# Performance work log

Measured on AMD Instinct MI355X. Metric: run time of the kernel, lower is better.

Reference implementation:

```python
import jax, jax.numpy as jnp
import numpy as np

B = 65536
IN_F = 1024
OUT_F = 1024


def setup_inputs() -> dict:
    key = jax.random.key(0)
    k1, k2 = jax.random.split(key)
    x = jax.random.normal(k1, (B, IN_F), dtype=jnp.float32)
    # init matches torch: normal(0, sqrt(2/(in+out)))
    std = np.sqrt(2.0 / (IN_F + OUT_F)).astype(np.float32)
    weight = jax.random.normal(k2, (OUT_F, IN_F), dtype=jnp.float32) * std
    bias = jnp.zeros((OUT_F,), dtype=jnp.float32)
    return {"x": x, "weight": weight, "bias": bias}


def reference(x, weight, bias):
    # Deterministic binarization: sign(w) in {-1, 0, +1} (sign(0)=0, same as torch)
    w_bin = jnp.sign(weight)
    # [B, in] @ [in, out] + [out]
    return jnp.matmul(x, w_bin.T) + bias[None, :]
```

## Files before the change

### kernel.cpp

```cpp
#include <hip/hip_runtime.h>


typedef __bf16 bf16x8 __attribute__((ext_vector_type(8)));
typedef __bf16 bf16x4 __attribute__((ext_vector_type(4)));
typedef float  f32x4  __attribute__((ext_vector_type(4)));

constexpr int Mdim = 65536, Ndim = 1024, Kdim = 1024;
constexpr int BM = 256, BN = 256, BK = 64;
constexpr int NKT = Kdim / BK;
constexpr int NWG = (Mdim / BM) * (Ndim / BN);

typedef const __attribute__((address_space(1))) char ga_char;
typedef __attribute__((address_space(3))) char lds_char;
__device__ __forceinline__ void gload16(const void* g, void* l) {
    __builtin_amdgcn_global_load_lds((ga_char*)g, (lds_char*)l, 16, 0, 0);
}
__device__ __forceinline__ f32x4 mfma16(bf16x8 a, bf16x8 b, f32x4 c) {
    return __builtin_amdgcn_mfma_f32_16x16x32_bf16(a, b, c, 0, 0, 0);
}

__global__ __launch_bounds__(256)
void wprep_kernel(const float* __restrict__ W, __bf16* __restrict__ WS) {
    const int id = blockIdx.x * 256 + threadIdx.x;
    const int c  = id & 7;
    const int kt = (id >> 3) & 15;
    const int n  = id >> 7;
    const float* src = W + (size_t)n * Kdim + kt * 64 + c * 8;
    f32x4 a = *(const f32x4*)src;
    f32x4 b = *(const f32x4*)(src + 4);
    bf16x8 o;
#pragma unroll
    for (int e = 0; e < 4; ++e) {
        o[e]     = (__bf16)(float)((a[e] > 0.f) - (a[e] < 0.f));
        o[e + 4] = (__bf16)(float)((b[e] > 0.f) - (b[e] < 0.f));
    }
    const int row  = n & 255;
    const int colb = n >> 8;
    __bf16* dst = WS + (size_t)(colb * 16 + kt) * 16384
                + row * 64 + ((c ^ (row & 7)) * 8);
    *(bf16x8*)dst = o;
}

__global__ __launch_bounds__(512, 2)
void binlin256(const float* __restrict__ X, const __bf16* __restrict__ WS,
               const float* __restrict__ bias, float* __restrict__ out)
{
    __shared__ __align__(16) __bf16 Al[2][BM * BK];
    __shared__ __align__(16) __bf16 Bl[2][BN * BK];

    const int swz  = (blockIdx.x & 7) * (NWG / 8) + (blockIdx.x >> 3);
    const int colb = swz & 3;
    const int rowb = swz >> 2;
    const int row0 = rowb * BM;

    const int tid  = threadIdx.x;
    const int lane = tid & 63;
    const int wid  = tid >> 6;
    const int wr   = wid >> 2;
    const int wcn  = wid & 3;
    const int fr   = lane & 15;
    const int hq   = lane >> 4;

    const int s_r = tid >> 4;
    const int s_c = tid & 15;
    const float* Xb = X + (size_t)(row0 + s_r) * Kdim + s_c * 4;

    const __bf16* WSb = WS + (size_t)colb * 16 * 16384;

    f32x4 ra[8];
    auto GLA = [&](int kt) {
        const float* p = Xb + kt * 64;
#pragma unroll
        for (int q = 0; q < 8; ++q)
            ra[q] = *(const f32x4*)(p + (size_t)(q * 32) * Kdim);
    };
    auto DSWA = [&](int buf) {
#pragma unroll
        for (int q = 0; q < 8; ++q) {
            bf16x4 v;
#pragma unroll
            for (int e = 0; e < 4; ++e) v[e] = (__bf16)ra[q][e];
            const int row  = q * 32 + s_r;
            const int byte = row * 128 + (((s_c >> 1) ^ (row & 7)) << 4)
                           + (s_c & 1) * 8;
            *(bf16x4*)((char*)&Al[buf][0] + byte) = v;
        }
    };
    auto STB = [&](int buf, int kt) {
        const __bf16* s0 = WSb + (size_t)kt * 16384 + wid * 2048 + lane * 8;
#pragma unroll
        for (int i = 0; i < 4; ++i)
            gload16(s0 + i * 512, &Bl[buf][wid * 2048 + i * 512]);
    };

    auto lda = [&](int buf, int i, int ks) -> bf16x8 {
        const int row  = wr * 128 + i * 16 + fr;
        const int byte = row * 128 + (((ks * 4 + hq) ^ (row & 7)) << 4);
        return *(const bf16x8*)((const char*)&Al[buf][0] + byte);
    };
    auto ldb = [&](int buf, int j, int ks) -> bf16x8 {
        const int row  = wcn * 64 + j * 16 + fr;
        const int byte = row * 128 + (((ks * 4 + hq) ^ (row & 7)) << 4);
        return *(const bf16x8*)((const char*)&Bl[buf][0] + byte);
    };

    f32x4 acc[8][4] = {};

    GLA(0);
    STB(0, 0);
    DSWA(0);
    __syncthreads();

    int cur = 0;
    for (int kt = 0; kt < NKT; ++kt) {
        const int nxt = cur ^ 1;
        const bool pre = (kt + 1 < NKT);
        if (pre) { GLA(kt + 1); STB(nxt, kt + 1); }

        bf16x8 a0[4], a1[4], b0[4], b1[4];

#pragma unroll
        for (int j = 0; j < 4; ++j) b0[j] = ldb(cur, j, 0);
#pragma unroll
        for (int i = 0; i < 4; ++i) a0[i] = lda(cur, i, 0);
        __builtin_amdgcn_s_setprio(1);
#pragma unroll
        for (int i = 0; i < 4; ++i)
#pragma unroll
            for (int j = 0; j < 4; ++j)
                acc[i][j] = mfma16(a0[i], b0[j], acc[i][j]);
        __builtin_amdgcn_s_setprio(0);

#pragma unroll
        for (int i = 0; i < 4; ++i) a1[i] = lda(cur, i + 4, 0);
        __builtin_amdgcn_s_setprio(1);
#pragma unroll
        for (int i = 0; i < 4; ++i)
#pragma unroll
            for (int j = 0; j < 4; ++j)
                acc[i + 4][j] = mfma16(a1[i], b0[j], acc[i + 4][j]);
        __builtin_amdgcn_s_setprio(0);

#pragma unroll
        for (int j = 0; j < 4; ++j) b1[j] = ldb(cur, j, 1);
#pragma unroll
        for (int i = 0; i < 4; ++i) a0[i] = lda(cur, i, 1);
        __builtin_amdgcn_s_setprio(1);
#pragma unroll
        for (int i = 0; i < 4; ++i)
#pragma unroll
            for (int j = 0; j < 4; ++j)
                acc[i][j] = mfma16(a0[i], b1[j], acc[i][j]);
        __builtin_amdgcn_s_setprio(0);

#pragma unroll
        for (int i = 0; i < 4; ++i) a1[i] = lda(cur, i + 4, 1);
        if (pre) DSWA(nxt);
        __builtin_amdgcn_s_setprio(1);
#pragma unroll
        for (int i = 0; i < 4; ++i)
#pragma unroll
            for (int j = 0; j < 4; ++j)
                acc[i + 4][j] = mfma16(a1[i], b1[j], acc[i + 4][j]);
        __builtin_amdgcn_s_setprio(0);

        __syncthreads();
        cur = nxt;
    }

    const int orow = row0 + wr * 128 + hq * 4;
    const int ocol = colb * 256 + wcn * 64 + fr;
#pragma unroll
    for (int j = 0; j < 4; ++j) {
        const float bv = bias[ocol + j * 16];
#pragma unroll
        for (int i = 0; i < 8; ++i)
#pragma unroll
            for (int r = 0; r < 4; ++r)
                out[(size_t)(orow + i * 16 + r) * Ndim + (ocol + j * 16)] =
                    acc[i][j][r] + bv;
    }
}

__global__ __launch_bounds__(256)
void binlin_fallback(const float* __restrict__ X, const float* __restrict__ Wf,
                     const float* __restrict__ bias, float* __restrict__ out)
{
    __shared__ __align__(16) __bf16 Al[2][128][32];
    __shared__ __align__(16) __bf16 Bl[2][128][32];
    constexpr int NT = Kdim / 32;
    const int swz  = (blockIdx.x & 7) * (4096 / 8) + (blockIdx.x >> 3);
    const int colb = swz & 7, rowb = swz >> 3;
    const int row0 = rowb * 128, col0 = colb * 128;
    const int tid = threadIdx.x, lane = tid & 63, wid = tid >> 6;
    const int wr = wid >> 1, wc = wid & 1;
    const int sr = tid >> 2, sc = (tid & 3) * 8;
    const float* Xb = X + (size_t)row0 * Kdim;
    const float* Wb = Wf + (size_t)col0 * Kdim;
    f32x4 ra[2][2], rb[2][2];
    auto GL = [&](int k0) {
#pragma unroll
        for (int p = 0; p < 2; ++p) {
            const float* sa = Xb + (size_t)(p * 64 + sr) * Kdim + k0 + sc;
            ra[p][0] = *(const f32x4*)sa; ra[p][1] = *(const f32x4*)(sa + 4);
            const float* sb = Wb + (size_t)(p * 64 + sr) * Kdim + k0 + sc;
            rb[p][0] = *(const f32x4*)sb; rb[p][1] = *(const f32x4*)(sb + 4);
        }
    };
    auto DSW = [&](int buf) {
#pragma unroll
        for (int p = 0; p < 2; ++p) {
            bf16x8 va, vb;
#pragma unroll
            for (int e = 0; e < 4; ++e) {
                va[e] = (__bf16)ra[p][0][e]; va[e + 4] = (__bf16)ra[p][1][e];
                float a = rb[p][0][e], b = rb[p][1][e];
                vb[e] = (__bf16)(float)((a > 0.f) - (a < 0.f));
                vb[e + 4] = (__bf16)(float)((b > 0.f) - (b < 0.f));
            }
            *(bf16x8*)&Al[buf][p * 64 + sr][sc] = va;
            *(bf16x8*)&Bl[buf][p * 64 + sr][sc] = vb;
        }
    };
    f32x4 acc[4][4] = {};
    const int fr = lane & 15, ks = (lane >> 4) * 8;
    auto COMP = [&](int buf) {
        bf16x8 af[4], bf[4];
#pragma unroll
        for (int i = 0; i < 4; ++i) af[i] = *(const bf16x8*)&Al[buf][wr * 64 + fr + i * 16][ks];
#pragma unroll
        for (int j = 0; j < 4; ++j) bf[j] = *(const bf16x8*)&Bl[buf][wc * 64 + fr + j * 16][ks];
#pragma unroll
        for (int i = 0; i < 4; ++i)
#pragma unroll
            for (int j = 0; j < 4; ++j)
                acc[i][j] = mfma16(af[i], bf[j], acc[i][j]);
    };
    GL(0); DSW(0); __syncthreads();
    int cur = 0;
    for (int t = 0; t < NT; ++t) {
        if (t + 1 < NT) GL((t + 1) * 32);
        COMP(cur);
        if (t + 1 < NT) { DSW(cur ^ 1); __syncthreads(); cur ^= 1; }
    }
    const int orow = row0 + wr * 64 + (lane >> 4) * 4;
    const int ocol = col0 + wc * 64 + fr;
#pragma unroll
    for (int j = 0; j < 4; ++j) {
        const float bv = bias[ocol + j * 16];
#pragma unroll
        for (int i = 0; i < 4; ++i)
#pragma unroll
            for (int r = 0; r < 4; ++r)
                out[(size_t)(orow + i * 16 + r) * Ndim + (ocol + j * 16)] = acc[i][j][r] + bv;
    }
}

extern "C" void kernel_launch(void* const* d_in, const int* in_sizes, int n_in,
                              void* d_out, int out_size, void* d_ws, size_t ws_size,
                              hipStream_t stream) {
    const float* x  = (const float*)d_in[0];
    const float* w  = (const float*)d_in[1];
    const float* b  = (const float*)d_in[2];
    float* out      = (float*)d_out;

    constexpr size_t WS_BYTES = (size_t)Ndim * Kdim * sizeof(__bf16);

    if (ws_size >= WS_BYTES) {
        __bf16* ws = (__bf16*)d_ws;
        wprep_kernel<<<dim3(512), dim3(256), 0, stream>>>(w, ws);
        binlin256<<<dim3(NWG), dim3(512), 0, stream>>>(x, ws, b, out);
    } else {
        binlin_fallback<<<dim3(4096), dim3(256), 0, stream>>>(x, w, b, out);
    }
}
```

Measured before the change: 239.1 us.

## Split A-tile prefetch into halves interleaved with MFMA phases and barriers

Reorganizes the fp32 X tile loads so each thread reads 64 contiguous bytes per row half, and splits the prefetch into two halves issued at different MFMA phases. The bf16 LDS stores now use 16-byte writes and are interleaved with the compute, with raw s_barrier between phases. The goal is to lower register pressure (8 staged vectors instead of 16 in flight at once, one shared A fragment array) and to spread global and LDS traffic more evenly across the loop. The cost is extra barriers per iteration and manual waitcnt handling, which could add stalls or hide ordering hazards.

```diff
diff --git a/kernel.cpp b/kernel.cpp
--- a/kernel.cpp
+++ b/kernel.cpp
@@ -18,6 +18,9 @@
 __device__ __forceinline__ f32x4 mfma16(bf16x8 a, bf16x8 b, f32x4 c) {
     return __builtin_amdgcn_mfma_f32_16x16x32_bf16(a, b, c, 0, 0, 0);
 }
+#define BARRIER()    asm volatile("s_barrier" ::: "memory")
+#define WAIT_VM0()   asm volatile("s_waitcnt vmcnt(0)" ::: "memory")
+#define WAIT_LGKM0() asm volatile("s_waitcnt lgkmcnt(0)" ::: "memory")
 
 __global__ __launch_bounds__(256)
 void wprep_kernel(const float* __restrict__ W, __bf16* __restrict__ WS) {
@@ -61,32 +64,40 @@
     const int fr   = lane & 15;
     const int hq   = lane >> 4;
 
-    const int s_r = tid >> 4;
-    const int s_c = tid & 15;
-    const float* Xb = X + (size_t)(row0 + s_r) * Kdim + s_c * 4;
+    const int a_r = tid >> 2;
+    const int a_c = (tid & 3) * 16;
+    const float* Xb = X + (size_t)(row0 + a_r) * Kdim + a_c;
 
     const __bf16* WSb = WS + (size_t)colb * 16 * 16384;
 
-    f32x4 ra[8];
-    auto GLA = [&](int kt) {
+    f32x4 rA0[4], rA1[4];
+
+    auto GLA0 = [&](int kt) {
         const float* p = Xb + kt * 64;
 #pragma unroll
-        for (int q = 0; q < 8; ++q)
-            ra[q] = *(const f32x4*)(p + (size_t)(q * 32) * Kdim);
-    };
-    auto DSWA = [&](int buf) {
-#pragma unroll
-        for (int q = 0; q < 8; ++q) {
-            bf16x4 v;
-#pragma unroll
-            for (int e = 0; e < 4; ++e) v[e] = (__bf16)ra[q][e];
-            const int row  = q * 32 + s_r;
-            const int byte = row * 128 + (((s_c >> 1) ^ (row & 7)) << 4)
-                           + (s_c & 1) * 8;
-            *(bf16x4*)((char*)&Al[buf][0] + byte) = v;
-        }
-    };
-    auto STB = [&](int buf, int kt) {
+        for (int q = 0; q < 4; ++q) rA0[q] = *(const f32x4*)(p + q * 4);
+    };
+    auto GLA1 = [&](int kt) {
+        const float* p = Xb + (size_t)128 * Kdim + kt * 64;
+#pragma unroll
+        for (int q = 0; q < 4; ++q) rA1[q] = *(const f32x4*)(p + q * 4);
+    };
+    auto DSWA = [&](int buf, int h, f32x4* r) {
+        const int row = h * 128 + a_r;
+#pragma unroll
+        for (int w = 0; w < 2; ++w) {
+            bf16x8 v;
+#pragma unroll
+            for (int e = 0; e < 4; ++e) {
+                v[e]     = (__bf16)r[w * 2][e];
+                v[e + 4] = (__bf16)r[w * 2 + 1][e];
+            }
+            const int c    = (a_c >> 3) + w;
+            const int byte = row * 128 + ((c ^ (row & 7)) << 4);
+            *(bf16x8*)((char*)&Al[buf][0] + byte) = v;
+        }
+    };
+    auto GLB = [&](int buf, int kt) {
         const __bf16* s0 = WSb + (size_t)kt * 16384 + wid * 2048 + lane * 8;
 #pragma unroll
         for (int i = 0; i < 4; ++i)
@@ -106,65 +117,71 @@
 
     f32x4 acc[8][4] = {};
 
-    GLA(0);
-    STB(0, 0);
-    DSWA(0);
+    GLA0(0); GLA1(0); GLB(0, 0);
+    DSWA(0, 0, rA0); DSWA(0, 1, rA1);
     __syncthreads();
 
     int cur = 0;
     for (int kt = 0; kt < NKT; ++kt) {
         const int nxt = cur ^ 1;
         const bool pre = (kt + 1 < NKT);
-        if (pre) { GLA(kt + 1); STB(nxt, kt + 1); }
-
-        bf16x8 a0[4], a1[4], b0[4], b1[4];
-
+        bf16x8 a[4], b0[4], b1[4];
+
+        if (pre) GLA0(kt + 1);
 #pragma unroll
         for (int j = 0; j < 4; ++j) b0[j] = ldb(cur, j, 0);
 #pragma unroll
-        for (int i = 0; i < 4; ++i) a0[i] = lda(cur, i, 0);
-        __builtin_amdgcn_s_setprio(1);
-#pragma unroll
-        for (int i = 0; i < 4; ++i)
-#pragma unroll
-            for (int j = 0; j < 4; ++j)
-                acc[i][j] = mfma16(a0[i], b0[j], acc[i][j]);
-        __builtin_amdgcn_s_setprio(0);
-
-#pragma unroll
-        for (int i = 0; i < 4; ++i) a1[i] = lda(cur, i + 4, 0);
-        __builtin_amdgcn_s_setprio(1);
-#pragma unroll
-        for (int i = 0; i < 4; ++i)
-#pragma unroll
-            for (int j = 0; j < 4; ++j)
-                acc[i + 4][j] = mfma16(a1[i], b0[j], acc[i + 4][j]);
-        __builtin_amdgcn_s_setprio(0);
-
+        for (int i = 0; i < 4; ++i) a[i] = lda(cur, i, 0);
+        __builtin_amdgcn_s_setprio(1);
+#pragma unroll
+        for (int i = 0; i < 4; ++i)
+#pragma unroll
+            for (int j = 0; j < 4; ++j)
+                acc[i][j] = mfma16(a[i], b0[j], acc[i][j]);
+        __builtin_amdgcn_s_setprio(0);
+        BARRIER();
+
+        if (pre) GLA1(kt + 1);
+#pragma unroll
+        for (int i = 0; i < 4; ++i) a[i] = lda(cur, i + 4, 0);
+        __builtin_amdgcn_s_setprio(1);
+#pragma unroll
+        for (int i = 0; i < 4; ++i)
+#pragma unroll
+            for (int j = 0; j < 4; ++j)
+                acc[i + 4][j] = mfma16(a[i], b0[j], acc[i + 4][j]);
+        __builtin_amdgcn_s_setprio(0);
+        BARRIER();
+
+        if (pre) { GLB(nxt, kt + 1); DSWA(nxt, 0, rA0); }
 #pragma unroll
         for (int j = 0; j < 4; ++j) b1[j] = ldb(cur, j, 1);
 #pragma unroll
-        for (int i = 0; i < 4; ++i) a0[i] = lda(cur, i, 1);
-        __builtin_amdgcn_s_setprio(1);
-#pragma unroll
-        for (int i = 0; i < 4; ++i)
-#pragma unroll
-            for (int j = 0; j < 4; ++j)
-                acc[i][j] = mfma16(a0[i], b1[j], acc[i][j]);
-        __builtin_amdgcn_s_setprio(0);
-
-#pragma unroll
-        for (int i = 0; i < 4; ++i) a1[i] = lda(cur, i + 4, 1);
-        if (pre) DSWA(nxt);
-        __builtin_amdgcn_s_setprio(1);
-#pragma unroll
-        for (int i = 0; i < 4; ++i)
-#pragma unroll
-            for (int j = 0; j < 4; ++j)
-                acc[i + 4][j] = mfma16(a1[i], b1[j], acc[i + 4][j]);
-        __builtin_amdgcn_s_setprio(0);
-
-        __syncthreads();
+        for (int i = 0; i < 4; ++i) a[i] = lda(cur, i, 1);
+        __builtin_amdgcn_s_setprio(1);
+#pragma unroll
+        for (int i = 0; i < 4; ++i)
+#pragma unroll
+            for (int j = 0; j < 4; ++j)
+                acc[i][j] = mfma16(a[i], b1[j], acc[i][j]);
+        __builtin_amdgcn_s_setprio(0);
+        BARRIER();
+
+        if (pre) DSWA(nxt, 1, rA1);
+#pragma unroll
+        for (int i = 0; i < 4; ++i) a[i] = lda(cur, i + 4, 1);
+        __builtin_amdgcn_s_setprio(1);
+#pragma unroll
+        for (int i = 0; i < 4; ++i)
+#pragma unroll
+            for (int j = 0; j < 4; ++j)
+                acc[i + 4][j] = mfma16(a[i], b1[j], acc[i + 4][j]);
+        __builtin_amdgcn_s_setprio(0);
+        if (pre) {
+            WAIT_LGKM0();
+            WAIT_VM0();
+        }
+        BARRIER();
         cur = nxt;
     }
 
```

Result: no change. 243.1 us (+1.7%).

## Shrink GEMM tile to 128x256x32 with MFMA-fragment-ordered weights

Applied to the files above, without the earlier changes.

Replaces the 256x256x64 tile kernel with a 128x256 tile and K-step of 32, launched with a higher occupancy hint (4 blocks per CU). The binarized weights are now pre-packed in MFMA fragment order, so each B fragment is one contiguous 16-byte LDS read without swizzling. The A tile uses padded 80-byte LDS rows instead of an XOR swizzle. The aim is more resident waves to hide the latency of loading and converting X. The cost is less compute per barrier, twice as many K iterations and synchronisations, and fewer MFMAs per wave per step.

```diff
diff --git a/kernel.cpp b/kernel.cpp
--- a/kernel.cpp
+++ b/kernel.cpp
@@ -2,13 +2,13 @@
 
 
 typedef __bf16 bf16x8 __attribute__((ext_vector_type(8)));
-typedef __bf16 bf16x4 __attribute__((ext_vector_type(4)));
 typedef float  f32x4  __attribute__((ext_vector_type(4)));
 
 constexpr int Mdim = 65536, Ndim = 1024, Kdim = 1024;
-constexpr int BM = 256, BN = 256, BK = 64;
+constexpr int BM = 128, BN = 256, BK = 32;
 constexpr int NKT = Kdim / BK;
 constexpr int NWG = (Mdim / BM) * (Ndim / BN);
+constexpr int AROWB = 80;
 
 typedef const __attribute__((address_space(1))) char ga_char;
 typedef __attribute__((address_space(3))) char lds_char;
@@ -21,11 +21,15 @@
 
 __global__ __launch_bounds__(256)
 void wprep_kernel(const float* __restrict__ W, __bf16* __restrict__ WS) {
-    const int id = blockIdx.x * 256 + threadIdx.x;
-    const int c  = id & 7;
-    const int kt = (id >> 3) & 15;
-    const int n  = id >> 7;
-    const float* src = W + (size_t)n * Kdim + kt * 64 + c * 8;
+    const int id   = blockIdx.x * 256 + threadIdx.x;
+    const int colb = id >> 15;
+    const int kt   = (id >> 10) & 31;
+    const int g    = id & 1023;
+    const int nb   = g >> 6;
+    const int lane = g & 63;
+    const int row  = colb * 256 + nb * 16 + (lane & 15);
+    const int col  = kt * 32 + (lane >> 4) * 8;
+    const float* src = W + (size_t)row * Kdim + col;
     f32x4 a = *(const f32x4*)src;
     f32x4 b = *(const f32x4*)(src + 4);
     bf16x8 o;
@@ -34,18 +38,14 @@
         o[e]     = (__bf16)(float)((a[e] > 0.f) - (a[e] < 0.f));
         o[e + 4] = (__bf16)(float)((b[e] > 0.f) - (b[e] < 0.f));
     }
-    const int row  = n & 255;
-    const int colb = n >> 8;
-    __bf16* dst = WS + (size_t)(colb * 16 + kt) * 16384
-                + row * 64 + ((c ^ (row & 7)) * 8);
-    *(bf16x8*)dst = o;
-}
-
-__global__ __launch_bounds__(512, 2)
-void binlin256(const float* __restrict__ X, const __bf16* __restrict__ WS,
-               const float* __restrict__ bias, float* __restrict__ out)
+    *(bf16x8*)(WS + (size_t)id * 8) = o;
+}
+
+__global__ __launch_bounds__(512, 4)
+void binlin128x256(const float* __restrict__ X, const __bf16* __restrict__ WS,
+                   const float* __restrict__ bias, float* __restrict__ out)
 {
-    __shared__ __align__(16) __bf16 Al[2][BM * BK];
+    __shared__ __align__(16) char Al[2][BM * AROWB];
     __shared__ __align__(16) __bf16 Bl[2][BN * BK];
 
     const int swz  = (blockIdx.x & 7) * (NWG / 8) + (blockIdx.x >> 3);
@@ -61,120 +61,80 @@
     const int fr   = lane & 15;
     const int hq   = lane >> 4;
 
-    const int s_r = tid >> 4;
-    const int s_c = tid & 15;
-    const float* Xb = X + (size_t)(row0 + s_r) * Kdim + s_c * 4;
-
-    const __bf16* WSb = WS + (size_t)colb * 16 * 16384;
-
-    f32x4 ra[8];
+    const int a_r = tid >> 2;
+    const int a_c = (tid & 3) * 8;
+    const float* Xb = X + (size_t)(row0 + a_r) * Kdim + a_c;
+
+    const __bf16* WSb = WS + (size_t)colb * (Ndim / BN == 4 ? 262144 : 262144);
+
+    f32x4 ra[2];
     auto GLA = [&](int kt) {
-        const float* p = Xb + kt * 64;
-#pragma unroll
-        for (int q = 0; q < 8; ++q)
-            ra[q] = *(const f32x4*)(p + (size_t)(q * 32) * Kdim);
+        const float* p = Xb + kt * BK;
+        ra[0] = *(const f32x4*)p;
+        ra[1] = *(const f32x4*)(p + 4);
     };
     auto DSWA = [&](int buf) {
-#pragma unroll
-        for (int q = 0; q < 8; ++q) {
-            bf16x4 v;
-#pragma unroll
-            for (int e = 0; e < 4; ++e) v[e] = (__bf16)ra[q][e];
-            const int row  = q * 32 + s_r;
-            const int byte = row * 128 + (((s_c >> 1) ^ (row & 7)) << 4)
-                           + (s_c & 1) * 8;
-            *(bf16x4*)((char*)&Al[buf][0] + byte) = v;
-        }
-    };
-    auto STB = [&](int buf, int kt) {
-        const __bf16* s0 = WSb + (size_t)kt * 16384 + wid * 2048 + lane * 8;
-#pragma unroll
-        for (int i = 0; i < 4; ++i)
-            gload16(s0 + i * 512, &Bl[buf][wid * 2048 + i * 512]);
-    };
-
-    auto lda = [&](int buf, int i, int ks) -> bf16x8 {
-        const int row  = wr * 128 + i * 16 + fr;
-        const int byte = row * 128 + (((ks * 4 + hq) ^ (row & 7)) << 4);
-        return *(const bf16x8*)((const char*)&Al[buf][0] + byte);
-    };
-    auto ldb = [&](int buf, int j, int ks) -> bf16x8 {
-        const int row  = wcn * 64 + j * 16 + fr;
-        const int byte = row * 128 + (((ks * 4 + hq) ^ (row & 7)) << 4);
-        return *(const bf16x8*)((const char*)&Bl[buf][0] + byte);
-    };
-
-    f32x4 acc[8][4] = {};
-
-    GLA(0);
-    STB(0, 0);
-    DSWA(0);
+        bf16x8 v;
+#pragma unroll
+        for (int e = 0; e < 4; ++e) {
+            v[e]     = (__bf16)ra[0][e];
+            v[e + 4] = (__bf16)ra[1][e];
+        }
+        *(bf16x8*)(&Al[buf][a_r * AROWB + a_c * 2]) = v;
+    };
+    auto GLB = [&](int buf, int kt) {
+        const __bf16* s = WSb + (size_t)kt * 8192 + wid * 1024 + lane * 8;
+        gload16(s,       &Bl[buf][wid * 1024]);
+        gload16(s + 512, &Bl[buf][wid * 1024 + 512]);
+    };
+
+    auto lda = [&](int buf, int i) -> bf16x8 {
+        const int row = wr * 64 + i * 16 + fr;
+        return *(const bf16x8*)(&Al[buf][row * AROWB + hq * 16]);
+    };
+    auto ldb = [&](int buf, int j) -> bf16x8 {
+        const int nb = wcn * 4 + j;
+        return *(const bf16x8*)(&Bl[buf][nb * 512 + lane * 8]);
+    };
+
+    f32x4 acc[4][4] = {};
+
+    GLA(0); GLB(0, 0); DSWA(0);
     __syncthreads();
 
     int cur = 0;
-    for (int kt = 0; kt < NKT; ++kt) {
+    for (int t = 0; t < NKT; ++t) {
         const int nxt = cur ^ 1;
-        const bool pre = (kt + 1 < NKT);
-        if (pre) { GLA(kt + 1); STB(nxt, kt + 1); }
-
-        bf16x8 a0[4], a1[4], b0[4], b1[4];
-
-#pragma unroll
-        for (int j = 0; j < 4; ++j) b0[j] = ldb(cur, j, 0);
-#pragma unroll
-        for (int i = 0; i < 4; ++i) a0[i] = lda(cur, i, 0);
+        const bool pre = (t + 1 < NKT);
+        if (pre) { GLA(t + 1); GLB(nxt, t + 1); }
+
+        bf16x8 af[4];
+#pragma unroll
+        for (int i = 0; i < 4; ++i) af[i] = lda(cur, i);
         __builtin_amdgcn_s_setprio(1);
 #pragma unroll
-        for (int i = 0; i < 4; ++i)
-#pragma unroll
-            for (int j = 0; j < 4; ++j)
-                acc[i][j] = mfma16(a0[i], b0[j], acc[i][j]);
+        for (int j = 0; j < 4; ++j) {
+            bf16x8 bf = ldb(cur, j);
+#pragma unroll
+            for (int i = 0; i < 4; ++i)
+                acc[i][j] = mfma16(af[i], bf, acc[i][j]);
+        }
         __builtin_amdgcn_s_setprio(0);
 
-#pragma unroll
-        for (int i = 0; i < 4; ++i) a1[i] = lda(cur, i + 4, 0);
-        __builtin_amdgcn_s_setprio(1);
-#pragma unroll
-        for (int i = 0; i < 4; ++i)
-#pragma unroll
-            for (int j = 0; j < 4; ++j)
-                acc[i + 4][j] = mfma16(a1[i], b0[j], acc[i + 4][j]);
-        __builtin_amdgcn_s_setprio(0);
-
-#pragma unroll
-        for (int j = 0; j < 4; ++j) b1[j] = ldb(cur, j, 1);
-#pragma unroll
-        for (int i = 0; i < 4; ++i) a0[i] = lda(cur, i, 1);
-        __builtin_amdgcn_s_setprio(1);
-#pragma unroll
-        for (int i = 0; i < 4; ++i)
-#pragma unroll
-            for (int j = 0; j < 4; ++j)
-                acc[i][j] = mfma16(a0[i], b1[j], acc[i][j]);
-        __builtin_amdgcn_s_setprio(0);
-
-#pragma unroll
-        for (int i = 0; i < 4; ++i) a1[i] = lda(cur, i + 4, 1);
-        if (pre) DSWA(nxt);
-        __builtin_amdgcn_s_setprio(1);
-#pragma unroll
-        for (int i = 0; i < 4; ++i)
-#pragma unroll
-            for (int j = 0; j < 4; ++j)
-                acc[i + 4][j] = mfma16(a1[i], b1[j], acc[i + 4][j]);
-        __builtin_amdgcn_s_setprio(0);
-
-        __syncthreads();
+        if (pre) {
+            DSWA(nxt);
+            __syncthreads();
+        }
         cur = nxt;
     }
 
-    const int orow = row0 + wr * 128 + hq * 4;
-    const int ocol = colb * 256 + wcn * 64 + fr;
+    const int orow = row0 + wr * 64 + hq * 4;
+    const int ocol = colb * BN + wcn * 64 + fr;
 #pragma unroll
     for (int j = 0; j < 4; ++j) {
         const float bv = bias[ocol + j * 16];
 #pragma unroll
-        for (int i = 0; i < 8; ++i)
+        for (int i = 0; i < 4; ++i)
 #pragma unroll
             for (int r = 0; r < 4; ++r)
                 out[(size_t)(orow + i * 16 + r) * Ndim + (ocol + j * 16)] =
@@ -269,7 +229,7 @@
     if (ws_size >= WS_BYTES) {
         __bf16* ws = (__bf16*)d_ws;
         wprep_kernel<<<dim3(512), dim3(256), 0, stream>>>(w, ws);
-        binlin256<<<dim3(NWG), dim3(512), 0, stream>>>(x, ws, b, out);
+        binlin128x256<<<dim3(NWG), dim3(512), 0, stream>>>(x, ws, b, out);
     } else {
         binlin_fallback<<<dim3(4096), dim3(256), 0, stream>>>(x, w, b, out);
     }
```

After: 233.5 us. 1.02x faster.
